# Kernel tuning notes

Hardware: AMD Instinct MI355X
Metric: run time of the kernel (lower is better)

The kernel has to match this reference:

```python
import jax, jax.numpy as jnp
import numpy as np

N, E = 50000, 800000
DIN, DH, DOUT = 128, 128, 64


def setup_inputs() -> dict:
    key = jax.random.key(0)
    k = jax.random.split(key, 6)
    node_features = jax.random.normal(k[0], (N, DIN), dtype=jnp.float32)
    edge_src = jax.random.randint(k[1], (E,), 0, N)
    edge_dst = jax.random.randint(k[2], (E,), 0, N)
    # Glorot-ish init for the two GCNConv weight matrices, zero bias (PyG default bias=True)
    W1 = jax.random.normal(k[3], (DIN, DH), dtype=jnp.float32) * (1.0 / np.sqrt(DIN))
    b1 = jnp.zeros((DH,), dtype=jnp.float32)
    W2 = jax.random.normal(k[4], (DH, DOUT), dtype=jnp.float32) * (1.0 / np.sqrt(DH))
    b2 = jnp.zeros((DOUT,), dtype=jnp.float32)
    return {"node_features": node_features, "edge_src": edge_src, "edge_dst": edge_dst,
            "W1": W1, "b1": b1, "W2": W2, "b2": b2}


def gcn_conv(x, W, b, src, dst, n):
    """PyG GCNConv: add self-loops, symmetric D^-1/2 (A+I) D^-1/2 normalization."""
    xw = x @ W  # [n, d_out]
    loops = jnp.arange(n, dtype=src.dtype)
    s = jnp.concatenate([src, loops])  # edges + self-loops
    d = jnp.concatenate([dst, loops])
    deg = jax.ops.segment_sum(jnp.ones_like(d, dtype=xw.dtype), d, num_segments=n)
    dinv = jnp.where(deg > 0, jax.lax.rsqrt(deg), 0.0)
    norm = dinv[s] * dinv[d]  # [E + n]
    msg = xw[s] * norm[:, None]  # gather + scale (memory-bound)
    out = jax.ops.segment_sum(msg, d, num_segments=n)  # scatter-add
    return out + b


def reference(node_features, edge_src, edge_dst, W1, b1, W2, b2):
    n = node_features.shape[0]
    h = gcn_conv(node_features, W1, b1, edge_src, edge_dst, n)
    h = jax.nn.relu(h)  # dropout omitted (inference / eval mode)
    h = gcn_conv(h, W2, b2, edge_src, edge_dst, n)
    # EdgePredictor: per-edge dot product of endpoint representations
    score = jnp.sum(h[edge_src] * h[edge_dst], axis=-1)  # [E]
    return score
```

## Files before the change

kernel.cpp:

```cpp
#include <hip/hip_runtime.h>
#include <hip/hip_bf16.h>
#include <type_traits>


#define DIN 128
#define DH  128
#define DOUT 64
#define CAP 8192

__device__ inline float2 bf2_to_f2(unsigned u) {
    union { unsigned i; float f; } a, b;
    a.i = u << 16;
    b.i = u & 0xffff0000u;
    return make_float2(a.f, b.f);
}
__device__ inline float bf_to_f(unsigned short u) {
    union { unsigned i; float f; } a;
    a.i = ((unsigned)u) << 16;
    return a.f;
}
__device__ inline unsigned short f_to_bf(float f) {
    union { float f; unsigned i; } v; v.f = f;
    unsigned r = v.i + 0x7fffu + ((v.i >> 16) & 1u);
    return (unsigned short)(r >> 16);
}

__global__ __launch_bounds__(256) void bucket_count_kernel(const int* __restrict__ dst,
                                                           int* __restrict__ gcnt,
                                                           int E, int nbuck) {
    __shared__ int hist[256];
    int t = threadIdx.x;
    hist[t] = 0;
    __syncthreads();
    int base = blockIdx.x * 4096 + t;
#pragma unroll
    for (int it = 0; it < 16; ++it) {
        int e = base + it * 256;
        if (e < E) atomicAdd(&hist[dst[e] >> 8], 1);
    }
    __syncthreads();
    if (t < nbuck && hist[t]) atomicAdd(&gcnt[t], hist[t]);
}

__global__ __launch_bounds__(256) void scan_buckets_kernel(const int* __restrict__ gcnt,
                                                           int* __restrict__ gbase,
                                                           int* __restrict__ gcursor,
                                                           int* __restrict__ row_ptr,
                                                           int nbuck, int N, int E) {
    __shared__ int lds[256];
    int t = threadIdx.x;
    int v = (t < nbuck) ? gcnt[t] : 0;
    lds[t] = v;
    __syncthreads();
    for (int off = 1; off < 256; off <<= 1) {
        int u = (t >= off) ? lds[t - off] : 0;
        __syncthreads();
        lds[t] += u;
        __syncthreads();
    }
    int ex = lds[t] - v;
    if (t < nbuck) { gbase[t] = ex; gcursor[t] = ex; }
    if (t == 0) { gbase[nbuck] = E; row_ptr[N] = E; }
}

__global__ __launch_bounds__(256) void bucket_place_kernel(const int* __restrict__ src,
                                                           const int* __restrict__ dst,
                                                           int* __restrict__ gcursor,
                                                           uint2* __restrict__ tmp,
                                                           int E, int nbuck) {
    __shared__ int hist[256];
    __shared__ int cur[256];
    int t = threadIdx.x;
    hist[t] = 0;
    __syncthreads();
    int base = blockIdx.x * 4096 + t;
    int d[16];
#pragma unroll
    for (int it = 0; it < 16; ++it) {
        int e = base + it * 256;
        d[it] = (e < E) ? dst[e] : -1;
        if (d[it] >= 0) atomicAdd(&hist[d[it] >> 8], 1);
    }
    __syncthreads();
    if (t < nbuck && hist[t]) cur[t] = atomicAdd(&gcursor[t], hist[t]);
    __syncthreads();
#pragma unroll
    for (int it = 0; it < 16; ++it) {
        int e = base + it * 256;
        if (d[it] >= 0) {
            int r = atomicAdd(&cur[d[it] >> 8], 1);
            tmp[r] = make_uint2((unsigned)src[e], (unsigned)d[it]);
        }
    }
}

__global__ __launch_bounds__(256) void bucket_csr_kernel(const uint2* __restrict__ tmp,
                                                         const int* __restrict__ gbase,
                                                         int* __restrict__ row_ptr,
                                                         float* __restrict__ dinv,
                                                         int* __restrict__ col, int N) {
    __shared__ int hist[256], cur[256], pfx[256];
    __shared__ unsigned esrc[CAP];
    __shared__ unsigned char eloc[CAP];
    __shared__ unsigned sorted[CAP];
    int b = blockIdx.x, t = threadIdx.x;
    int beg = gbase[b], end = gbase[b + 1];
    int size = end - beg;
    if (size > CAP) size = CAP;
    hist[t] = 0;
    __syncthreads();
    for (int i = t; i < size; i += 256) {
        uint2 e = tmp[beg + i];
        esrc[i] = e.x;
        int loc = e.y & 255;
        eloc[i] = (unsigned char)loc;
        atomicAdd(&hist[loc], 1);
    }
    __syncthreads();
    int v = hist[t];
    pfx[t] = v;
    __syncthreads();
    for (int off = 1; off < 256; off <<= 1) {
        int u = (t >= off) ? pfx[t - off] : 0;
        __syncthreads();
        pfx[t] += u;
        __syncthreads();
    }
    int ex = pfx[t] - v;
    cur[t] = ex;
    int node = b * 256 + t;
    if (node < N) {
        row_ptr[node] = beg + ex;
        dinv[node] = rsqrtf((float)(v + 1));
    }
    __syncthreads();
    for (int i = t; i < size; i += 256) {
        int r = atomicAdd(&cur[eloc[i]], 1);
        sorted[r] = esrc[i];
    }
    __syncthreads();
    for (int i = t; i < size; i += 256) col[beg + i] = (int)sorted[i];
}

template <int COLS, typename XT>
__global__ __launch_bounds__(256) void gemm_kernel(const XT* __restrict__ X,
                                                   const float* __restrict__ W,
                                                   const float* __restrict__ dinv,
                                                   unsigned short* __restrict__ Y,
                                                   int nrows) {
    constexpr int CPT = COLS / 16;
    __shared__ float Xs[16][132];
    __shared__ float Ws[16][COLS];
    int tid = threadIdx.x;
    int tx = tid & 15;
    int ty = tid >> 4;
    int row0 = blockIdx.x * 128;

    float acc[8][CPT];
#pragma unroll
    for (int i = 0; i < 8; ++i)
#pragma unroll
        for (int j = 0; j < CPT; ++j) acc[i][j] = 0.f;

    for (int kc = 0; kc < 128; kc += 16) {
        __syncthreads();
        if constexpr (std::is_same_v<XT, float>) {
#pragma unroll
            for (int it = 0; it < 2; ++it) {
                int idx = tid + it * 256;
                int r = idx >> 2;
                int kk = (idx & 3) * 4;
                int gr = row0 + r; if (gr >= nrows) gr = nrows - 1;
                float4 v = *(const float4*)(X + (size_t)gr * 128 + kc + kk);
                Xs[kk + 0][r] = v.x; Xs[kk + 1][r] = v.y;
                Xs[kk + 2][r] = v.z; Xs[kk + 3][r] = v.w;
            }
        } else {
            int r = tid >> 1;
            int kk = (tid & 1) * 8;
            int gr = row0 + r; if (gr >= nrows) gr = nrows - 1;
            uint4 u = *(const uint4*)(X + (size_t)gr * 128 + kc + kk);
            float2 p;
            p = bf2_to_f2(u.x); Xs[kk + 0][r] = p.x; Xs[kk + 1][r] = p.y;
            p = bf2_to_f2(u.y); Xs[kk + 2][r] = p.x; Xs[kk + 3][r] = p.y;
            p = bf2_to_f2(u.z); Xs[kk + 4][r] = p.x; Xs[kk + 5][r] = p.y;
            p = bf2_to_f2(u.w); Xs[kk + 6][r] = p.x; Xs[kk + 7][r] = p.y;
        }
#pragma unroll
        for (int idx = tid; idx < 16 * COLS / 4; idx += 256) {
            int kr = idx / (COLS / 4);
            int c4 = idx % (COLS / 4);
            *(float4*)&Ws[kr][c4 * 4] =
                *(const float4*)(W + (size_t)(kc + kr) * COLS + c4 * 4);
        }
        __syncthreads();
#pragma unroll
        for (int k = 0; k < 16; ++k) {
            float a[8];
            *(float4*)&a[0] = *(const float4*)&Xs[k][ty * 8];
            *(float4*)&a[4] = *(const float4*)&Xs[k][ty * 8 + 4];
            float b[CPT];
            *(float4*)&b[0] = *(const float4*)&Ws[k][tx * 4];
            if constexpr (CPT == 8)
                *(float4*)&b[4] = *(const float4*)&Ws[k][64 + tx * 4];
#pragma unroll
            for (int i = 0; i < 8; ++i)
#pragma unroll
                for (int j = 0; j < CPT; ++j)
                    acc[i][j] = fmaf(a[i], b[j], acc[i][j]);
        }
    }
#pragma unroll
    for (int i = 0; i < 8; ++i) {
        int gr = row0 + ty * 8 + i;
        if (gr >= nrows) continue;
        float dv = dinv[gr];
        ushort4 o;
        o.x = f_to_bf(acc[i][0] * dv); o.y = f_to_bf(acc[i][1] * dv);
        o.z = f_to_bf(acc[i][2] * dv); o.w = f_to_bf(acc[i][3] * dv);
        *(ushort4*)(Y + (size_t)gr * COLS + tx * 4) = o;
        if constexpr (CPT == 8) {
            ushort4 o2;
            o2.x = f_to_bf(acc[i][4] * dv); o2.y = f_to_bf(acc[i][5] * dv);
            o2.z = f_to_bf(acc[i][6] * dv); o2.w = f_to_bf(acc[i][7] * dv);
            *(ushort4*)(Y + (size_t)gr * COLS + 64 + tx * 4) = o2;
        }
    }
}

template <int D, bool RELU>
__global__ __launch_bounds__(256) void agg_kernel(const unsigned short* __restrict__ y,
                                                  const int* __restrict__ row_ptr,
                                                  const int* __restrict__ col,
                                                  const float* __restrict__ dinv,
                                                  const float* __restrict__ bias,
                                                  unsigned short* __restrict__ out, int n) {
    constexpr int V = D / 64;
    int w = (blockIdx.x * 256 + threadIdx.x) >> 6;
    int lane = threadIdx.x & 63;
    if (w >= n) return;
    float acc[V];
    if constexpr (V == 2) {
        float2 t = bf2_to_f2(*(const unsigned*)(y + (size_t)w * D + lane * 2));
        acc[0] = t.x; acc[1] = t.y;
    } else {
        acc[0] = bf_to_f(y[(size_t)w * D + lane]);
    }
    int beg = row_ptr[w], end = row_ptr[w + 1];
    int i = beg;
    for (; i + 8 <= end; i += 8) {
        int s[8];
#pragma unroll
        for (int u = 0; u < 8; ++u) s[u] = col[i + u];
        if constexpr (V == 2) {
            unsigned tv[8];
#pragma unroll
            for (int u = 0; u < 8; ++u)
                tv[u] = *(const unsigned*)(y + (size_t)s[u] * D + lane * 2);
#pragma unroll
            for (int u = 0; u < 8; ++u) {
                float2 f = bf2_to_f2(tv[u]);
                acc[0] += f.x; acc[1] += f.y;
            }
        } else {
            unsigned short tv[8];
#pragma unroll
            for (int u = 0; u < 8; ++u) tv[u] = y[(size_t)s[u] * D + lane];
#pragma unroll
            for (int u = 0; u < 8; ++u) acc[0] += bf_to_f(tv[u]);
        }
    }
    for (; i < end; ++i) {
        int s = col[i];
        if constexpr (V == 2) {
            float2 f = bf2_to_f2(*(const unsigned*)(y + (size_t)s * D + lane * 2));
            acc[0] += f.x; acc[1] += f.y;
        } else {
            acc[0] += bf_to_f(y[(size_t)s * D + lane]);
        }
    }
    float dv = dinv[w];
    if constexpr (V == 2) {
        float r0 = fmaf(dv, acc[0], bias[lane * 2]);
        float r1 = fmaf(dv, acc[1], bias[lane * 2 + 1]);
        if (RELU) { r0 = fmaxf(r0, 0.f); r1 = fmaxf(r1, 0.f); }
        unsigned pk = (unsigned)f_to_bf(r0) | ((unsigned)f_to_bf(r1) << 16);
        *(unsigned*)(out + (size_t)w * D + lane * 2) = pk;
    } else {
        float r = fmaf(dv, acc[0], bias[lane]);
        if (RELU) r = fmaxf(r, 0.f);
        out[(size_t)w * D + lane] = f_to_bf(r);
    }
}

__global__ __launch_bounds__(256) void score_kernel(const unsigned short* __restrict__ h2,
                                                    const int* __restrict__ src,
                                                    const int* __restrict__ dst,
                                                    float* __restrict__ out, int E) {
    int tid = blockIdx.x * 256 + threadIdx.x;
    int e = tid >> 4;
    if (e >= E) return;
    int q = tid & 15;
    int s = src[e], d = dst[e];
    uint2 ua = *(const uint2*)(h2 + (size_t)s * 64 + q * 4);
    uint2 ub = *(const uint2*)(h2 + (size_t)d * 64 + q * 4);
    float2 a0 = bf2_to_f2(ua.x), a1 = bf2_to_f2(ua.y);
    float2 b0 = bf2_to_f2(ub.x), b1 = bf2_to_f2(ub.y);
    float v = a0.x * b0.x + a0.y * b0.y + a1.x * b1.x + a1.y * b1.y;
    v += __shfl_xor(v, 8);
    v += __shfl_xor(v, 4);
    v += __shfl_xor(v, 2);
    v += __shfl_xor(v, 1);
    if (q == 0) out[e] = v;
}

extern "C" void kernel_launch(void* const* d_in, const int* in_sizes, int n_in,
                              void* d_out, int out_size, void* d_ws, size_t ws_size,
                              hipStream_t stream) {
    const float* X   = (const float*)d_in[0];
    const int*   src = (const int*)d_in[1];
    const int*   dst = (const int*)d_in[2];
    const float* W1  = (const float*)d_in[3];
    const float* b1  = (const float*)d_in[4];
    const float* W2  = (const float*)d_in[5];
    const float* b2  = (const float*)d_in[6];
    float* score = (float*)d_out;

    const int N = in_sizes[0] / DIN;
    const int E = in_sizes[1];
    const int nbuck = (N + 255) / 256;
    const int EB = (E + 4095) / 4096;

    auto align = [](size_t x) { return (x + 255) & ~(size_t)255; };
    char* p = (char*)d_ws;
    int*   gcnt    = (int*)p;               p += align(256 * 4);
    int*   gbase   = (int*)p;               p += align(257 * 4);
    int*   gcursor = (int*)p;               p += align(256 * 4);
    int*   row_ptr = (int*)p;               p += align((size_t)(N + 1) * 4);
    float* dinv    = (float*)p;             p += align((size_t)N * 4);
    int*   col     = (int*)p;               p += align((size_t)E * 4);
    uint2* tmp     = (uint2*)p;             p += align((size_t)E * 8);
    unsigned short* y1 = (unsigned short*)p; p += align((size_t)N * DH * 2);
    unsigned short* h1 = (unsigned short*)p; p += align((size_t)N * DH * 2);
    unsigned short* y2 = y1;
    unsigned short* h2 = y1 + (size_t)N * DOUT;

    hipMemsetAsync(gcnt, 0, 256 * 4, stream);

    bucket_count_kernel<<<EB, 256, 0, stream>>>(dst, gcnt, E, nbuck);
    scan_buckets_kernel<<<1, 256, 0, stream>>>(gcnt, gbase, gcursor, row_ptr, nbuck, N, E);
    bucket_place_kernel<<<EB, 256, 0, stream>>>(src, dst, gcursor, tmp, E, nbuck);
    bucket_csr_kernel<<<nbuck, 256, 0, stream>>>(tmp, gbase, row_ptr, dinv, col, N);

    int gemm_blocks = (N + 127) / 128;
    gemm_kernel<DH, float><<<gemm_blocks, 256, 0, stream>>>(X, W1, dinv, y1, N);

    int agg_blocks = (N + 3) / 4;
    agg_kernel<DH, true><<<agg_blocks, 256, 0, stream>>>(y1, row_ptr, col, dinv, b1, h1, N);

    gemm_kernel<DOUT, unsigned short><<<gemm_blocks, 256, 0, stream>>>(h1, W2, dinv, y2, N);
    agg_kernel<DOUT, false><<<agg_blocks, 256, 0, stream>>>(y2, row_ptr, col, dinv, b2, h2, N);

    int score_blocks = (E * 16 + 255) / 256;
    score_kernel<<<score_blocks, 256, 0, stream>>>(h2, src, dst, score, E);
}
```

Measured before the change: 269.4 us.

## Replace FP32 SIMT GEMMs with bf16 MFMA matrix-core kernel

Both dense transforms (X@W1 and h1@W2) now use a kernel that loads the full 128-row tile and transposed weights into shared memory as bf16, then computes with mfma_f32_16x16x32_bf16 instead of scalar FMAs. This moves the GEMM compute off the vector ALUs onto the matrix cores. It adds extra precision loss because X and W are rounded to bf16 before the multiply. It also brings a larger shared-memory footprint, scalar bf16 stores on output, and strided uncoalesced weight loads per block.

```diff
diff --git a/kernel.cpp b/kernel.cpp
--- a/kernel.cpp
+++ b/kernel.cpp
@@ -7,6 +7,9 @@
 #define DH  128
 #define DOUT 64
 #define CAP 8192
+
+typedef __attribute__((ext_vector_type(8))) short short8;
+typedef __attribute__((ext_vector_type(4))) float floatx4;
 
 __device__ inline float2 bf2_to_f2(unsigned u) {
     union { unsigned i; float f; } a, b;
@@ -143,87 +146,95 @@
 }
 
 template <int COLS, typename XT>
-__global__ __launch_bounds__(256) void gemm_kernel(const XT* __restrict__ X,
-                                                   const float* __restrict__ W,
-                                                   const float* __restrict__ dinv,
-                                                   unsigned short* __restrict__ Y,
-                                                   int nrows) {
-    constexpr int CPT = COLS / 16;
-    __shared__ float Xs[16][132];
-    __shared__ float Ws[16][COLS];
+__global__ __launch_bounds__(256) void mfma_gemm_kernel(const XT* __restrict__ X,
+                                                        const float* __restrict__ W,
+                                                        const float* __restrict__ dinv,
+                                                        unsigned short* __restrict__ Y,
+                                                        int nrows) {
+    constexpr int KP = 136;
+    __shared__ unsigned short Xs[128 * KP];
+    __shared__ unsigned short Wt[COLS * KP];
     int tid = threadIdx.x;
-    int tx = tid & 15;
-    int ty = tid >> 4;
     int row0 = blockIdx.x * 128;
 
-    float acc[8][CPT];
-#pragma unroll
-    for (int i = 0; i < 8; ++i)
-#pragma unroll
-        for (int j = 0; j < CPT; ++j) acc[i][j] = 0.f;
-
-    for (int kc = 0; kc < 128; kc += 16) {
-        __syncthreads();
-        if constexpr (std::is_same_v<XT, float>) {
-#pragma unroll
-            for (int it = 0; it < 2; ++it) {
-                int idx = tid + it * 256;
-                int r = idx >> 2;
-                int kk = (idx & 3) * 4;
-                int gr = row0 + r; if (gr >= nrows) gr = nrows - 1;
-                float4 v = *(const float4*)(X + (size_t)gr * 128 + kc + kk);
-                Xs[kk + 0][r] = v.x; Xs[kk + 1][r] = v.y;
-                Xs[kk + 2][r] = v.z; Xs[kk + 3][r] = v.w;
-            }
-        } else {
-            int r = tid >> 1;
-            int kk = (tid & 1) * 8;
+    if constexpr (std::is_same_v<XT, float>) {
+#pragma unroll
+        for (int it = 0; it < 16; ++it) {
+            int idx = it * 256 + tid;
+            int r = idx >> 5;
+            int c4 = (idx & 31) * 4;
             int gr = row0 + r; if (gr >= nrows) gr = nrows - 1;
-            uint4 u = *(const uint4*)(X + (size_t)gr * 128 + kc + kk);
-            float2 p;
-            p = bf2_to_f2(u.x); Xs[kk + 0][r] = p.x; Xs[kk + 1][r] = p.y;
-            p = bf2_to_f2(u.y); Xs[kk + 2][r] = p.x; Xs[kk + 3][r] = p.y;
-            p = bf2_to_f2(u.z); Xs[kk + 4][r] = p.x; Xs[kk + 5][r] = p.y;
-            p = bf2_to_f2(u.w); Xs[kk + 6][r] = p.x; Xs[kk + 7][r] = p.y;
-        }
-#pragma unroll
-        for (int idx = tid; idx < 16 * COLS / 4; idx += 256) {
-            int kr = idx / (COLS / 4);
-            int c4 = idx % (COLS / 4);
-            *(float4*)&Ws[kr][c4 * 4] =
-                *(const float4*)(W + (size_t)(kc + kr) * COLS + c4 * 4);
-        }
-        __syncthreads();
-#pragma unroll
-        for (int k = 0; k < 16; ++k) {
-            float a[8];
-            *(float4*)&a[0] = *(const float4*)&Xs[k][ty * 8];
-            *(float4*)&a[4] = *(const float4*)&Xs[k][ty * 8 + 4];
-            float b[CPT];
-            *(float4*)&b[0] = *(const float4*)&Ws[k][tx * 4];
-            if constexpr (CPT == 8)
-                *(float4*)&b[4] = *(const float4*)&Ws[k][64 + tx * 4];
-#pragma unroll
-            for (int i = 0; i < 8; ++i)
-#pragma unroll
-                for (int j = 0; j < CPT; ++j)
-                    acc[i][j] = fmaf(a[i], b[j], acc[i][j]);
-        }
-    }
-#pragma unroll
-    for (int i = 0; i < 8; ++i) {
-        int gr = row0 + ty * 8 + i;
-        if (gr >= nrows) continue;
-        float dv = dinv[gr];
-        ushort4 o;
-        o.x = f_to_bf(acc[i][0] * dv); o.y = f_to_bf(acc[i][1] * dv);
-        o.z = f_to_bf(acc[i][2] * dv); o.w = f_to_bf(acc[i][3] * dv);
-        *(ushort4*)(Y + (size_t)gr * COLS + tx * 4) = o;
-        if constexpr (CPT == 8) {
-            ushort4 o2;
-            o2.x = f_to_bf(acc[i][4] * dv); o2.y = f_to_bf(acc[i][5] * dv);
-            o2.z = f_to_bf(acc[i][6] * dv); o2.w = f_to_bf(acc[i][7] * dv);
-            *(ushort4*)(Y + (size_t)gr * COLS + 64 + tx * 4) = o2;
+            float4 v = *(const float4*)(X + (size_t)gr * 128 + c4);
+            ushort4 p;
+            p.x = f_to_bf(v.x); p.y = f_to_bf(v.y);
+            p.z = f_to_bf(v.z); p.w = f_to_bf(v.w);
+            *(ushort4*)&Xs[r * KP + c4] = p;
+        }
+    } else {
+#pragma unroll
+        for (int it = 0; it < 8; ++it) {
+            int idx = it * 256 + tid;
+            int r = idx >> 4;
+            int c8 = (idx & 15) * 8;
+            int gr = row0 + r; if (gr >= nrows) gr = nrows - 1;
+            uint4 v = *(const uint4*)(X + (size_t)gr * 128 + c8);
+            *(uint4*)&Xs[r * KP + c8] = v;
+        }
+    }
+#pragma unroll
+    for (int it = 0; it < COLS / 8; ++it) {
+        int idx = it * 256 + tid;
+        int n = idx >> 5;
+        int k4 = (idx & 31) * 4;
+        ushort4 p;
+        p.x = f_to_bf(W[(size_t)(k4 + 0) * COLS + n]);
+        p.y = f_to_bf(W[(size_t)(k4 + 1) * COLS + n]);
+        p.z = f_to_bf(W[(size_t)(k4 + 2) * COLS + n]);
+        p.w = f_to_bf(W[(size_t)(k4 + 3) * COLS + n]);
+        *(ushort4*)&Wt[n * KP + k4] = p;
+    }
+    __syncthreads();
+
+    constexpr int CT = COLS / 16;
+    int wv = tid >> 6, lane = tid & 63;
+    int lr = lane & 15;
+    int lk = (lane >> 4) * 8;
+    int rw = wv * 32;
+
+    floatx4 acc[2][CT];
+#pragma unroll
+    for (int rt = 0; rt < 2; ++rt)
+#pragma unroll
+        for (int ct = 0; ct < CT; ++ct) acc[rt][ct] = (floatx4){0.f, 0.f, 0.f, 0.f};
+
+#pragma unroll
+    for (int kk = 0; kk < 128; kk += 32) {
+        short8 a[2], b[CT];
+#pragma unroll
+        for (int rt = 0; rt < 2; ++rt)
+            a[rt] = *(const short8*)&Xs[(rw + rt * 16 + lr) * KP + kk + lk];
+#pragma unroll
+        for (int ct = 0; ct < CT; ++ct)
+            b[ct] = *(const short8*)&Wt[(ct * 16 + lr) * KP + kk + lk];
+#pragma unroll
+        for (int rt = 0; rt < 2; ++rt)
+#pragma unroll
+            for (int ct = 0; ct < CT; ++ct)
+                acc[rt][ct] = __builtin_amdgcn_mfma_f32_16x16x32_bf16(
+                    a[rt], b[ct], acc[rt][ct], 0, 0, 0);
+    }
+
+#pragma unroll
+    for (int rt = 0; rt < 2; ++rt) {
+#pragma unroll
+        for (int i = 0; i < 4; ++i) {
+            int grow = row0 + rw + rt * 16 + (lane >> 4) * 4 + i;
+            if (grow >= nrows) continue;
+            float dv = dinv[grow];
+#pragma unroll
+            for (int ct = 0; ct < CT; ++ct)
+                Y[(size_t)grow * COLS + ct * 16 + lr] =
+                    f_to_bf(acc[rt][ct][i] * dv);
         }
     }
 }
@@ -353,12 +364,12 @@
     bucket_csr_kernel<<<nbuck, 256, 0, stream>>>(tmp, gbase, row_ptr, dinv, col, N);
 
     int gemm_blocks = (N + 127) / 128;
-    gemm_kernel<DH, float><<<gemm_blocks, 256, 0, stream>>>(X, W1, dinv, y1, N);
+    mfma_gemm_kernel<DH, float><<<gemm_blocks, 256, 0, stream>>>(X, W1, dinv, y1, N);
 
     int agg_blocks = (N + 3) / 4;
     agg_kernel<DH, true><<<agg_blocks, 256, 0, stream>>>(y1, row_ptr, col, dinv, b1, h1, N);
 
-    gemm_kernel<DOUT, unsigned short><<<gemm_blocks, 256, 0, stream>>>(h1, W2, dinv, y2, N);
+    mfma_gemm_kernel<DOUT, unsigned short><<<gemm_blocks, 256, 0, stream>>>(h1, W2, dinv, y2, N);
     agg_kernel<DOUT, false><<<agg_blocks, 256, 0, stream>>>(y2, row_ptr, col, dinv, b2, h2, N);
 
     int score_blocks = (E * 16 + 255) / 256;
```

New measurement: 261.1 us. 3.1% less time.
